# Kernel tuning notes

Hardware: AMD Instinct MI355X
Metric: run time of the kernel (lower is better)

The kernel has to match this reference:

```python
import jax, jax.numpy as jnp
import numpy as np

N_NODES = 100000
N_EDGES = 1600000
MSG_DIM = 16
HID_DIM = 16
N_ETYPE = 16
N_CLASSES = 64


def setup_inputs() -> dict:
    key = jax.random.key(0)
    ks = jax.random.split(key, 11)
    s = 1.0 / np.sqrt(HID_DIM)
    return {
        "features": jax.random.normal(ks[0], (N_NODES, HID_DIM), dtype=jnp.float32),
        "src": jax.random.randint(ks[1], (N_EDGES,), 0, N_NODES, dtype=jnp.int32),
        "dst": jax.random.randint(ks[2], (N_EDGES,), 0, N_NODES, dtype=jnp.int32),
        "e_type": jax.random.randint(ks[3], (N_EDGES,), 0, N_ETYPE, dtype=jnp.int32),
        "edge_emb": jax.random.normal(ks[4], (N_ETYPE, MSG_DIM * HID_DIM), dtype=jnp.float32),
        "W_ih": jax.random.uniform(ks[5], (3 * HID_DIM, MSG_DIM), dtype=jnp.float32, minval=-s, maxval=s),
        "W_hh": jax.random.uniform(ks[6], (3 * HID_DIM, HID_DIM), dtype=jnp.float32, minval=-s, maxval=s),
        "b_ih": jax.random.uniform(ks[7], (3 * HID_DIM,), dtype=jnp.float32, minval=-s, maxval=s),
        "b_hh": jax.random.uniform(ks[8], (3 * HID_DIM,), dtype=jnp.float32, minval=-s, maxval=s),
        "W_out": jax.random.normal(ks[9], (N_CLASSES, HID_DIM), dtype=jnp.float32) * s,
        "b_out": jax.random.normal(ks[10], (N_CLASSES,), dtype=jnp.float32) * 0.01,
    }


def reference(features, src, dst, e_type, edge_emb, W_ih, W_hh, b_ih, b_hh, W_out, b_out):
    # Per-edge message: A_e @ h_src, A_e = edge-type embedding reshaped [msg, hid]
    A = edge_emb[e_type].reshape(-1, MSG_DIM, HID_DIM)          # [E, M, H]
    msg = jnp.einsum("emh,eh->em", A, features[src])            # [E, M]
    # Sum-aggregate messages into destination nodes
    m = jax.ops.segment_sum(msg, dst, num_segments=N_NODES)     # [N, M]
    # Single-step GRU (PyTorch gate order: r, z, n)
    gx = m @ W_ih.T + b_ih                                      # [N, 3H]
    gh = features @ W_hh.T + b_hh                               # [N, 3H]
    xr, xz, xn = jnp.split(gx, 3, axis=-1)
    hr, hz, hn = jnp.split(gh, 3, axis=-1)
    r = jax.nn.sigmoid(xr + hr)
    z = jax.nn.sigmoid(xz + hz)
    n = jnp.tanh(xn + r * hn)
    h = (1.0 - z) * n + z * features                            # [N, H]
    return h @ W_out.T + b_out                                  # [N, C]
```

## Files before the change

### kernel.cpp

```cpp
#include <hip/hip_runtime.h>

#define NNODES 100000
#define NEDGES 1600000
#define HID 16
#define MSG 16
#define NTYPE 16
#define NCLS 64

#define BSH 7
#define NBK ((NNODES + 127) >> 7)
#define CHSZ 8192
#define NCH ((NEDGES + CHSZ - 1) / CHSZ)
#define M_SCAN (NBK * NCH)
#define SCH 1024
#define NSB ((M_SCAN + SCH - 1) / SCH)

#define ASTR 20
#define ATY  320

#define RECCAP 2560
#define CHUNK 16
#define NCHK ((NEDGES + CHUNK - 1) / CHUNK)
#define AGG2_BLOCKS ((NCHK + 15) / 16)

__device__ __forceinline__ float sigmoid_f(float x) {
    return 1.0f / (1.0f + __expf(-x));
}
__device__ __forceinline__ float tanh_f(float x) {
    x = fminf(fmaxf(x, -15.0f), 15.0f);
    float e = __expf(2.0f * x);
    return (e - 1.0f) / (e + 1.0f);
}

__global__ __launch_bounds__(1024) void hist_k(const int* __restrict__ dst,
                                               int* __restrict__ cntmat) {
    __shared__ int cnt[NBK];
    const int t = threadIdx.x, ch = blockIdx.x;
    for (int b = t; b < NBK; b += 1024) cnt[b] = 0;
    __syncthreads();
    #pragma unroll
    for (int k = 0; k < CHSZ / 1024; k++) {
        int e = ch * CHSZ + k * 1024 + t;
        if (e < NEDGES) atomicAdd(&cnt[dst[e] >> BSH], 1);
    }
    __syncthreads();
    for (int b = t; b < NBK; b += 1024) cntmat[b * NCH + ch] = cnt[b];
}

__global__ __launch_bounds__(256) void scan_bsum(const int* __restrict__ x,
                                                 int* __restrict__ bsum) {
    const int t = threadIdx.x;
    int base = blockIdx.x * SCH + t * 4;
    int s = 0;
    #pragma unroll
    for (int q = 0; q < 4; q++) {
        int idx = base + q;
        if (idx < M_SCAN) s += x[idx];
    }
    #pragma unroll
    for (int d = 32; d > 0; d >>= 1) s += __shfl_down(s, d, 64);
    __shared__ int ws[4];
    int lane = t & 63, w = t >> 6;
    if (lane == 0) ws[w] = s;
    __syncthreads();
    if (t == 0) bsum[blockIdx.x] = ws[0] + ws[1] + ws[2] + ws[3];
}

__global__ __launch_bounds__(256) void scan_top(int* __restrict__ bsum) {
    const int t = threadIdx.x;
    int v = (t < NSB) ? bsum[t] : 0;
    int lane = t & 63, w = t >> 6;
    int s = v;
    #pragma unroll
    for (int d = 1; d < 64; d <<= 1) {
        int u = __shfl_up(s, d, 64);
        if (lane >= d) s += u;
    }
    __shared__ int ws[4];
    if (lane == 63) ws[w] = s;
    __syncthreads();
    int base = 0;
    #pragma unroll
    for (int q = 0; q < 4; q++) if (q < w) base += ws[q];
    if (t < NSB) bsum[t] = base + s - v;
}

__global__ __launch_bounds__(256) void scan_write(const int* __restrict__ bsum,
                                                  int* __restrict__ x) {
    const int t = threadIdx.x;
    int base = blockIdx.x * SCH + t * 4;
    int v[4]; int ts = 0;
    #pragma unroll
    for (int q = 0; q < 4; q++) {
        int idx = base + q;
        v[q] = (idx < M_SCAN) ? x[idx] : 0;
        ts += v[q];
    }
    int lane = t & 63, w = t >> 6;
    int s = ts;
    #pragma unroll
    for (int d = 1; d < 64; d <<= 1) {
        int u = __shfl_up(s, d, 64);
        if (lane >= d) s += u;
    }
    __shared__ int ws[4];
    if (lane == 63) ws[w] = s;
    __syncthreads();
    int wbase = 0;
    #pragma unroll
    for (int q = 0; q < 4; q++) if (q < w) wbase += ws[q];
    int run = bsum[blockIdx.x] + wbase + (s - ts);
    #pragma unroll
    for (int q = 0; q < 4; q++) {
        int idx = base + q;
        if (idx < M_SCAN) x[idx] = run;
        run += v[q];
    }
}

__global__ __launch_bounds__(1024) void scatter_k(const int* __restrict__ src,
                                                  const int* __restrict__ dst,
                                                  const int* __restrict__ et,
                                                  const int* __restrict__ offmat,
                                                  int* __restrict__ rec) {
    __shared__ int offc[NBK];
    const int t = threadIdx.x, ch = blockIdx.x;
    for (int b = t; b < NBK; b += 1024) offc[b] = offmat[b * NCH + ch];
    __syncthreads();
    #pragma unroll
    for (int k = 0; k < CHSZ / 1024; k++) {
        int e = ch * CHSZ + k * 1024 + t;
        if (e < NEDGES) {
            int d = dst[e];
            int b = d >> BSH;
            int pos = atomicAdd(&offc[b], 1);
            rec[pos] = src[e] | (et[e] << 17) | ((d & 127) << 21);
        }
    }
}

__global__ __launch_bounds__(256) void bnd_k(const int* __restrict__ offmat,
                                             int* __restrict__ bnd) {
    int k = blockIdx.x * 256 + threadIdx.x;
    if (k < NBK) bnd[k] = offmat[k * NCH];
    if (k == NBK) bnd[k] = NEDGES;
}

__global__ __launch_bounds__(256) void sort2_k(const int* __restrict__ offmat,
                                               int* __restrict__ rec) {
    __shared__ int buf[RECCAP];
    __shared__ int cnt[128];
    __shared__ int basec[128];
    __shared__ int wtot[4];
    const int t = threadIdx.x, b = blockIdx.x;
    const int jb = offmat[b * NCH];
    const int je = (b == NBK - 1) ? NEDGES : offmat[(b + 1) * NCH];
    const int len = je - jb;
    if (len <= 0 || len > RECCAP) return;

    if (t < 128) cnt[t] = 0;
    for (int k = t; k < len; k += 256) buf[k] = rec[jb + k];
    __syncthreads();
    for (int k = t; k < len; k += 256) atomicAdd(&cnt[((unsigned)buf[k]) >> 21], 1);
    __syncthreads();
    int v = (t < 128) ? cnt[t] : 0;
    int lane = t & 63, w = t >> 6;
    int s = v;
    #pragma unroll
    for (int d = 1; d < 64; d <<= 1) {
        int u = __shfl_up(s, d, 64);
        if (lane >= d) s += u;
    }
    if (lane == 63) wtot[w] = s;
    __syncthreads();
    if (t < 128) basec[t] = s - v + (w == 1 ? wtot[0] : 0);
    __syncthreads();
    for (int k = t; k < len; k += 256) {
        int r = buf[k];
        int p = atomicAdd(&basec[((unsigned)r) >> 21], 1);
        rec[jb + p] = r;
    }
}

__device__ __forceinline__ float dot16(const float4* A, float4 f0, float4 f1,
                                       float4 f2, float4 f3) {
    float4 A0 = A[0], A1 = A[1], A2 = A[2], A3 = A[3];
    float m;
    m  = A0.x*f0.x + A0.y*f0.y + A0.z*f0.z + A0.w*f0.w;
    m += A1.x*f1.x + A1.y*f1.y + A1.z*f1.z + A1.w*f1.w;
    m += A2.x*f2.x + A2.y*f2.y + A2.z*f2.z + A2.w*f2.w;
    m += A3.x*f3.x + A3.y*f3.y + A3.z*f3.z + A3.w*f3.w;
    return m;
}

__global__ __launch_bounds__(256) void agg2_k(const float* __restrict__ feat,
                                              const int* __restrict__ rec,
                                              const int* __restrict__ bnd_g,
                                              const float* __restrict__ edge_emb,
                                              float* __restrict__ magg) {
    __shared__ float At2[NTYPE * ATY];
    __shared__ int bnd[NBK + 1];
    const int t = threadIdx.x;
    #pragma unroll
    for (int idx = t; idx < NTYPE * MSG * HID; idx += 256) {
        int ty = idx >> 8, rem = idx & 255, ii = rem >> 4, h = rem & 15;
        At2[ty * ATY + ii * ASTR + h] = edge_emb[idx];
    }
    for (int k = t; k < NBK + 1; k += 256) bnd[k] = bnd_g[k];
    __syncthreads();

    const int g = t >> 4, i = t & 15;
    const int chunk = blockIdx.x * 16 + g;
    if (chunk >= NCHK) return;
    const int j0 = chunk * CHUNK;
    const int jend = (j0 + CHUNK < NEDGES) ? j0 + CHUNK : NEDGES;

    int lo = 0, hi = NBK;
    while (hi - lo > 1) {
        int mid = (lo + hi) >> 1;
        if (bnd[mid] <= j0) lo = mid; else hi = mid;
    }
    int b = lo, bnext = bnd[b + 1];

    float macc = 0.0f;
    int cur = -1;
    int j = j0;
    while (j < jend) {
        const bool has2 = (j + 1 < jend);
        int r1 = rec[j];
        int r2 = has2 ? rec[j + 1] : r1;
        const float4* p1 = (const float4*)(feat + (size_t)(r1 & 0x1FFFF) * HID);
        const float4* p2 = (const float4*)(feat + (size_t)(r2 & 0x1FFFF) * HID);
        float4 Fa0 = p1[0], Fa1 = p1[1], Fa2 = p1[2], Fa3 = p1[3];
        float4 Fb0 = p2[0], Fb1 = p2[1], Fb2 = p2[2], Fb3 = p2[3];
        __builtin_amdgcn_sched_barrier(0);

        while (j >= bnext) { ++b; bnext = bnd[b + 1]; }
        {
            int d1  = (b << BSH) | (((unsigned)r1) >> 21);
            int ty1 = (r1 >> 17) & 15;
            float m1 = dot16((const float4*)(At2 + ty1 * ATY + i * ASTR),
                             Fa0, Fa1, Fa2, Fa3);
            if (d1 != cur) {
                if (cur >= 0) atomicAdd(&magg[(size_t)cur * MSG + i], macc);
                macc = 0.0f; cur = d1;
            }
            macc += m1;
        }
        if (has2) {
            while (j + 1 >= bnext) { ++b; bnext = bnd[b + 1]; }
            int d2  = (b << BSH) | (((unsigned)r2) >> 21);
            int ty2 = (r2 >> 17) & 15;
            float m2 = dot16((const float4*)(At2 + ty2 * ATY + i * ASTR),
                             Fb0, Fb1, Fb2, Fb3);
            if (d2 != cur) {
                atomicAdd(&magg[(size_t)cur * MSG + i], macc);
                macc = 0.0f; cur = d2;
            }
            macc += m2;
        }
        j += 2;
    }
    if (cur >= 0) atomicAdd(&magg[(size_t)cur * MSG + i], macc);
}

__global__ __launch_bounds__(256) void ggnn_edge(
    const float* __restrict__ feat,
    const int* __restrict__ src,
    const int* __restrict__ dst,
    const int* __restrict__ etype,
    const float* __restrict__ edge_emb,
    float* __restrict__ magg)
{
    __shared__ float At[NTYPE * MSG * HID];
    for (int idx = threadIdx.x; idx < NTYPE * MSG * HID; idx += 256) {
        int ty = idx >> 8, rem = idx & 255, i = rem >> 4, hh = rem & 15;
        At[(ty << 8) | (hh << 4) | i] = edge_emb[idx];
    }
    __syncthreads();
    const long long total = (long long)NEDGES * MSG;
    for (long long w = (long long)blockIdx.x * 256 + threadIdx.x; w < total;
         w += (long long)gridDim.x * 256) {
        const int e = (int)(w >> 4);
        const int i = (int)(w & 15);
        const int s = src[e];
        const int d = dst[e];
        const int ty = etype[e];
        const float4* fp = (const float4*)(feat + (size_t)s * HID);
        const float4 f0 = fp[0], f1 = fp[1], f2 = fp[2], f3 = fp[3];
        const float* a = At + (ty << 8) + i;
        float m;
        m  = a[0*16]*f0.x + a[1*16]*f0.y + a[2*16]*f0.z + a[3*16]*f0.w;
        m += a[4*16]*f1.x + a[5*16]*f1.y + a[6*16]*f1.z + a[7*16]*f1.w;
        m += a[8*16]*f2.x + a[9*16]*f2.y + a[10*16]*f2.z + a[11*16]*f2.w;
        m += a[12*16]*f3.x + a[13*16]*f3.y + a[14*16]*f3.z + a[15*16]*f3.w;
        atomicAdd(magg + (size_t)d * MSG + i, m);
    }
}

__global__ __launch_bounds__(256) void node_k(
    const float* __restrict__ feat,
    const float* __restrict__ magg,
    const float* __restrict__ W_ih,
    const float* __restrict__ W_hh,
    const float* __restrict__ b_ih,
    const float* __restrict__ b_hh,
    const float* __restrict__ W_out,
    const float* __restrict__ b_out,
    float* __restrict__ out)
{
    __shared__ float hn_s[256 * 20];
    const int t = threadIdx.x;
    const int n = blockIdx.x * 256 + t;
    if (n < NNODES) {
        float hv[HID], mv[MSG];
        const float4* hp = (const float4*)(feat + (size_t)n * HID);
        const float4* mp = (const float4*)(magg + (size_t)n * MSG);
        #pragma unroll
        for (int q = 0; q < 4; q++) {
            float4 a = hp[q];
            hv[4*q+0] = a.x; hv[4*q+1] = a.y; hv[4*q+2] = a.z; hv[4*q+3] = a.w;
            float4 c = mp[q];
            mv[4*q+0] = c.x; mv[4*q+1] = c.y; mv[4*q+2] = c.z; mv[4*q+3] = c.w;
        }
        #pragma unroll
        for (int i = 0; i < HID; i++) {
            float xr = b_ih[i], xz = b_ih[16 + i], xn = b_ih[32 + i];
            float hr = b_hh[i], hz = b_hh[16 + i], hn = b_hh[32 + i];
            #pragma unroll
            for (int j = 0; j < HID; j++) {
                xr += W_ih[(i)      * 16 + j] * mv[j];
                xz += W_ih[(16 + i) * 16 + j] * mv[j];
                xn += W_ih[(32 + i) * 16 + j] * mv[j];
                hr += W_hh[(i)      * 16 + j] * hv[j];
                hz += W_hh[(16 + i) * 16 + j] * hv[j];
                hn += W_hh[(32 + i) * 16 + j] * hv[j];
            }
            float r  = sigmoid_f(xr + hr);
            float z  = sigmoid_f(xz + hz);
            float nn = tanh_f(xn + r * hn);
            hn_s[t * 20 + i] = (1.0f - z) * nn + z * hv[i];
        }
    }
    __syncthreads();

    const int w = t >> 6, g = (t >> 4) & 3, li = t & 15;
    float4 w4[4][4];
    #pragma unroll
    for (int rr = 0; rr < 4; rr++)
        #pragma unroll
        for (int qq = 0; qq < 4; qq++)
            w4[rr][qq] = ((const float4*)W_out)[(4 * li + rr) * 4 + qq];
    const float4 bo4 = ((const float4*)b_out)[li];
    const int nb = blockIdx.x * 256;

    #pragma unroll
    for (int it = 0; it < 16; it++) {
        int ln = it * 16 + w * 4 + g;
        int n2 = nb + ln;
        if (n2 < NNODES) {
            const float4* hq = (const float4*)(hn_s + ln * 20);
            float4 h0 = hq[0], h1 = hq[1], h2 = hq[2], h3 = hq[3];
            float4 o;
            o.x = bo4.x + w4[0][0].x*h0.x + w4[0][0].y*h0.y + w4[0][0].z*h0.z + w4[0][0].w*h0.w
                        + w4[0][1].x*h1.x + w4[0][1].y*h1.y + w4[0][1].z*h1.z + w4[0][1].w*h1.w
                        + w4[0][2].x*h2.x + w4[0][2].y*h2.y + w4[0][2].z*h2.z + w4[0][2].w*h2.w
                        + w4[0][3].x*h3.x + w4[0][3].y*h3.y + w4[0][3].z*h3.z + w4[0][3].w*h3.w;
            o.y = bo4.y + w4[1][0].x*h0.x + w4[1][0].y*h0.y + w4[1][0].z*h0.z + w4[1][0].w*h0.w
                        + w4[1][1].x*h1.x + w4[1][1].y*h1.y + w4[1][1].z*h1.z + w4[1][1].w*h1.w
                        + w4[1][2].x*h2.x + w4[1][2].y*h2.y + w4[1][2].z*h2.z + w4[1][2].w*h2.w
                        + w4[1][3].x*h3.x + w4[1][3].y*h3.y + w4[1][3].z*h3.z + w4[1][3].w*h3.w;
            o.z = bo4.z + w4[2][0].x*h0.x + w4[2][0].y*h0.y + w4[2][0].z*h0.z + w4[2][0].w*h0.w
                        + w4[2][1].x*h1.x + w4[2][1].y*h1.y + w4[2][1].z*h1.z + w4[2][1].w*h1.w
                        + w4[2][2].x*h2.x + w4[2][2].y*h2.y + w4[2][2].z*h2.z + w4[2][2].w*h2.w
                        + w4[2][3].x*h3.x + w4[2][3].y*h3.y + w4[2][3].z*h3.z + w4[2][3].w*h3.w;
            o.w = bo4.w + w4[3][0].x*h0.x + w4[3][0].y*h0.y + w4[3][0].z*h0.z + w4[3][0].w*h0.w
                        + w4[3][1].x*h1.x + w4[3][1].y*h1.y + w4[3][1].z*h1.z + w4[3][1].w*h1.w
                        + w4[3][2].x*h2.x + w4[3][2].y*h2.y + w4[3][2].z*h2.z + w4[3][2].w*h2.w
                        + w4[3][3].x*h3.x + w4[3][3].y*h3.y + w4[3][3].z*h3.z + w4[3][3].w*h3.w;
            ((float4*)(out + (size_t)n2 * NCLS))[li] = o;
        }
    }
}

extern "C" void kernel_launch(void* const* d_in, const int* in_sizes, int n_in,
                              void* d_out, int out_size, void* d_ws, size_t ws_size,
                              hipStream_t stream) {
    const float* feat     = (const float*)d_in[0];
    const int*   src      = (const int*)d_in[1];
    const int*   dst      = (const int*)d_in[2];
    const int*   etype    = (const int*)d_in[3];
    const float* edge_emb = (const float*)d_in[4];
    const float* W_ih     = (const float*)d_in[5];
    const float* W_hh     = (const float*)d_in[6];
    const float* b_ih     = (const float*)d_in[7];
    const float* b_hh     = (const float*)d_in[8];
    const float* W_out    = (const float*)d_in[9];
    const float* b_out    = (const float*)d_in[10];
    float* out = (float*)d_out;

    float* magg   = (float*)d_ws;
    int*   offmat = (int*)d_ws + (size_t)NNODES * MSG;
    int*   bsum   = offmat + M_SCAN;
    int*   bnd    = bsum + 256;
    int*   rec    = bnd + 1024;
    size_t need   = ((size_t)NNODES * MSG + M_SCAN + 256 + 1024 + NEDGES) * 4;

    hipMemsetAsync(magg, 0, (size_t)NNODES * MSG * sizeof(float), stream);
    if (ws_size >= need) {
        hist_k    <<<NCH, 1024, 0, stream>>>(dst, offmat);
        scan_bsum <<<NSB, 256, 0, stream>>>(offmat, bsum);
        scan_top  <<<1, 256, 0, stream>>>(bsum);
        scan_write<<<NSB, 256, 0, stream>>>(bsum, offmat);
        scatter_k <<<NCH, 1024, 0, stream>>>(src, dst, etype, offmat, rec);
        bnd_k     <<<4, 256, 0, stream>>>(offmat, bnd);
        sort2_k   <<<NBK, 256, 0, stream>>>(offmat, rec);
        agg2_k    <<<AGG2_BLOCKS, 256, 0, stream>>>(feat, rec, bnd, edge_emb, magg);
    } else {
        ggnn_edge<<<2560, 256, 0, stream>>>(feat, src, dst, etype, edge_emb, magg);
    }
    node_k<<<(NNODES + 255) / 256, 256, 0, stream>>>(
        feat, magg, W_ih, W_hh, b_ih, b_hh, W_out, b_out, out);
}
```

Measured before the change: 158.7 us.

## Fuse scan-top and bnd kernels, precompute chunk-bucket map, stage records in LDS

Drops the single-block scan_top launch by having each scan_write block reduce the preceding block sums itself, and writes bucket boundaries there, which removes the bnd_k launch. sort2_k now also fills a chunk-to-bucket table, so agg2_k no longer copies the boundary array into shared memory or binary-searches it. agg2_k stages its 256 records in LDS and runs a fixed 8-iteration loop that assumes the edge count divides evenly by the chunk size. The cost is a redundant partial reduction in every scan block and an extra workspace array.

```diff
diff --git a/kernel.cpp b/kernel.cpp
--- a/kernel.cpp
+++ b/kernel.cpp
@@ -20,8 +20,8 @@
 
 #define RECCAP 2560
 #define CHUNK 16
-#define NCHK ((NEDGES + CHUNK - 1) / CHUNK)
-#define AGG2_BLOCKS ((NCHK + 15) / 16)
+#define NCHK (NEDGES / CHUNK)
+#define AGG2_BLOCKS (NCHK / 16)
 
 __device__ __forceinline__ float sigmoid_f(float x) {
     return 1.0f / (1.0f + __expf(-x));
@@ -66,28 +66,23 @@
     if (t == 0) bsum[blockIdx.x] = ws[0] + ws[1] + ws[2] + ws[3];
 }
 
-__global__ __launch_bounds__(256) void scan_top(int* __restrict__ bsum) {
+__global__ __launch_bounds__(256) void scan_write(const int* __restrict__ bsum,
+                                                  int* __restrict__ x,
+                                                  int* __restrict__ bnd) {
     const int t = threadIdx.x;
-    int v = (t < NSB) ? bsum[t] : 0;
-    int lane = t & 63, w = t >> 6;
-    int s = v;
-    #pragma unroll
-    for (int d = 1; d < 64; d <<= 1) {
-        int u = __shfl_up(s, d, 64);
-        if (lane >= d) s += u;
-    }
-    __shared__ int ws[4];
-    if (lane == 63) ws[w] = s;
-    __syncthreads();
-    int base = 0;
-    #pragma unroll
-    for (int q = 0; q < 4; q++) if (q < w) base += ws[q];
-    if (t < NSB) bsum[t] = base + s - v;
-}
-
-__global__ __launch_bounds__(256) void scan_write(const int* __restrict__ bsum,
-                                                  int* __restrict__ x) {
-    const int t = threadIdx.x;
+    __shared__ int wsA[4];
+    __shared__ int bpref_s;
+    {
+        int v = (t < blockIdx.x && t < NSB) ? bsum[t] : 0;
+        #pragma unroll
+        for (int d = 32; d > 0; d >>= 1) v += __shfl_down(v, d, 64);
+        int lane = t & 63, w = t >> 6;
+        if (lane == 0) wsA[w] = v;
+        __syncthreads();
+        if (t == 0) bpref_s = wsA[0] + wsA[1] + wsA[2] + wsA[3];
+        __syncthreads();
+    }
+
     int base = blockIdx.x * SCH + t * 4;
     int v[4]; int ts = 0;
     #pragma unroll
@@ -103,19 +98,23 @@
         int u = __shfl_up(s, d, 64);
         if (lane >= d) s += u;
     }
-    __shared__ int ws[4];
-    if (lane == 63) ws[w] = s;
+    __shared__ int wsB[4];
+    if (lane == 63) wsB[w] = s;
     __syncthreads();
     int wbase = 0;
     #pragma unroll
-    for (int q = 0; q < 4; q++) if (q < w) wbase += ws[q];
-    int run = bsum[blockIdx.x] + wbase + (s - ts);
+    for (int q = 0; q < 4; q++) if (q < w) wbase += wsB[q];
+    int run = bpref_s + wbase + (s - ts);
     #pragma unroll
     for (int q = 0; q < 4; q++) {
         int idx = base + q;
-        if (idx < M_SCAN) x[idx] = run;
+        if (idx < M_SCAN) {
+            x[idx] = run;
+            if (idx % NCH == 0) bnd[idx / NCH] = run;
+        }
         run += v[q];
     }
+    if (blockIdx.x == 0 && t == 0) bnd[NBK] = NEDGES;
 }
 
 __global__ __launch_bounds__(1024) void scatter_k(const int* __restrict__ src,
@@ -139,47 +138,46 @@
     }
 }
 
-__global__ __launch_bounds__(256) void bnd_k(const int* __restrict__ offmat,
-                                             int* __restrict__ bnd) {
-    int k = blockIdx.x * 256 + threadIdx.x;
-    if (k < NBK) bnd[k] = offmat[k * NCH];
-    if (k == NBK) bnd[k] = NEDGES;
-}
-
-__global__ __launch_bounds__(256) void sort2_k(const int* __restrict__ offmat,
-                                               int* __restrict__ rec) {
+__global__ __launch_bounds__(256) void sort2_k(const int* __restrict__ bnd,
+                                               int* __restrict__ rec,
+                                               int* __restrict__ cb) {
     __shared__ int buf[RECCAP];
     __shared__ int cnt[128];
     __shared__ int basec[128];
     __shared__ int wtot[4];
     const int t = threadIdx.x, b = blockIdx.x;
-    const int jb = offmat[b * NCH];
-    const int je = (b == NBK - 1) ? NEDGES : offmat[(b + 1) * NCH];
+    const int jb = bnd[b];
+    const int je = bnd[b + 1];
     const int len = je - jb;
-    if (len <= 0 || len > RECCAP) return;
-
-    if (t < 128) cnt[t] = 0;
-    for (int k = t; k < len; k += 256) buf[k] = rec[jb + k];
-    __syncthreads();
-    for (int k = t; k < len; k += 256) atomicAdd(&cnt[((unsigned)buf[k]) >> 21], 1);
-    __syncthreads();
-    int v = (t < 128) ? cnt[t] : 0;
-    int lane = t & 63, w = t >> 6;
-    int s = v;
-    #pragma unroll
-    for (int d = 1; d < 64; d <<= 1) {
-        int u = __shfl_up(s, d, 64);
-        if (lane >= d) s += u;
-    }
-    if (lane == 63) wtot[w] = s;
-    __syncthreads();
-    if (t < 128) basec[t] = s - v + (w == 1 ? wtot[0] : 0);
-    __syncthreads();
-    for (int k = t; k < len; k += 256) {
-        int r = buf[k];
-        int p = atomicAdd(&basec[((unsigned)r) >> 21], 1);
-        rec[jb + p] = r;
-    }
+
+    if (len > 0 && len <= RECCAP) {
+        if (t < 128) cnt[t] = 0;
+        for (int k = t; k < len; k += 256) buf[k] = rec[jb + k];
+        __syncthreads();
+        for (int k = t; k < len; k += 256) atomicAdd(&cnt[((unsigned)buf[k]) >> 21], 1);
+        __syncthreads();
+        int v = (t < 128) ? cnt[t] : 0;
+        int lane = t & 63, w = t >> 6;
+        int s = v;
+        #pragma unroll
+        for (int d = 1; d < 64; d <<= 1) {
+            int u = __shfl_up(s, d, 64);
+            if (lane >= d) s += u;
+        }
+        if (lane == 63) wtot[w] = s;
+        __syncthreads();
+        if (t < 128) basec[t] = s - v + (w == 1 ? wtot[0] : 0);
+        __syncthreads();
+        for (int k = t; k < len; k += 256) {
+            int r = buf[k];
+            int p = atomicAdd(&basec[((unsigned)r) >> 21], 1);
+            rec[jb + p] = r;
+        }
+    }
+
+    const int c0 = (jb + CHUNK - 1) >> 4;
+    const int c1 = (je + CHUNK - 1) >> 4;
+    for (int c = c0 + t; c < c1; c += 256) cb[c] = b;
 }
 
 __device__ __forceinline__ float dot16(const float4* A, float4 f0, float4 f1,
@@ -195,73 +193,63 @@
 
 __global__ __launch_bounds__(256) void agg2_k(const float* __restrict__ feat,
                                               const int* __restrict__ rec,
-                                              const int* __restrict__ bnd_g,
+                                              const int* __restrict__ bnd,
+                                              const int* __restrict__ cb,
                                               const float* __restrict__ edge_emb,
                                               float* __restrict__ magg) {
     __shared__ float At2[NTYPE * ATY];
-    __shared__ int bnd[NBK + 1];
+    __shared__ int recs[256];
     const int t = threadIdx.x;
     #pragma unroll
     for (int idx = t; idx < NTYPE * MSG * HID; idx += 256) {
         int ty = idx >> 8, rem = idx & 255, ii = rem >> 4, h = rem & 15;
         At2[ty * ATY + ii * ASTR + h] = edge_emb[idx];
     }
-    for (int k = t; k < NBK + 1; k += 256) bnd[k] = bnd_g[k];
+    recs[t] = rec[blockIdx.x * 256 + t];
     __syncthreads();
 
     const int g = t >> 4, i = t & 15;
     const int chunk = blockIdx.x * 16 + g;
-    if (chunk >= NCHK) return;
-    const int j0 = chunk * CHUNK;
-    const int jend = (j0 + CHUNK < NEDGES) ? j0 + CHUNK : NEDGES;
-
-    int lo = 0, hi = NBK;
-    while (hi - lo > 1) {
-        int mid = (lo + hi) >> 1;
-        if (bnd[mid] <= j0) lo = mid; else hi = mid;
-    }
-    int b = lo, bnext = bnd[b + 1];
+    const int jbase = chunk << 4;
+    const int lbase = g << 4;
+
+    int b = cb[chunk];
+    int bnext = bnd[b + 1];
 
     float macc = 0.0f;
     int cur = -1;
-    int j = j0;
-    while (j < jend) {
-        const bool has2 = (j + 1 < jend);
-        int r1 = rec[j];
-        int r2 = has2 ? rec[j + 1] : r1;
+    #pragma unroll 1
+    for (int p = 0; p < 8; p++) {
+        int r1 = recs[lbase + 2 * p];
+        int r2 = recs[lbase + 2 * p + 1];
         const float4* p1 = (const float4*)(feat + (size_t)(r1 & 0x1FFFF) * HID);
         const float4* p2 = (const float4*)(feat + (size_t)(r2 & 0x1FFFF) * HID);
         float4 Fa0 = p1[0], Fa1 = p1[1], Fa2 = p1[2], Fa3 = p1[3];
         float4 Fb0 = p2[0], Fb1 = p2[1], Fb2 = p2[2], Fb3 = p2[3];
         __builtin_amdgcn_sched_barrier(0);
 
+        int j = jbase + 2 * p;
         while (j >= bnext) { ++b; bnext = bnd[b + 1]; }
-        {
-            int d1  = (b << BSH) | (((unsigned)r1) >> 21);
-            int ty1 = (r1 >> 17) & 15;
-            float m1 = dot16((const float4*)(At2 + ty1 * ATY + i * ASTR),
-                             Fa0, Fa1, Fa2, Fa3);
-            if (d1 != cur) {
-                if (cur >= 0) atomicAdd(&magg[(size_t)cur * MSG + i], macc);
-                macc = 0.0f; cur = d1;
-            }
-            macc += m1;
-        }
-        if (has2) {
-            while (j + 1 >= bnext) { ++b; bnext = bnd[b + 1]; }
-            int d2  = (b << BSH) | (((unsigned)r2) >> 21);
-            int ty2 = (r2 >> 17) & 15;
-            float m2 = dot16((const float4*)(At2 + ty2 * ATY + i * ASTR),
-                             Fb0, Fb1, Fb2, Fb3);
-            if (d2 != cur) {
-                atomicAdd(&magg[(size_t)cur * MSG + i], macc);
-                macc = 0.0f; cur = d2;
-            }
-            macc += m2;
-        }
-        j += 2;
-    }
-    if (cur >= 0) atomicAdd(&magg[(size_t)cur * MSG + i], macc);
+        int d1 = (b << BSH) | (((unsigned)r1) >> 21);
+        float m1 = dot16((const float4*)(At2 + ((r1 >> 17) & 15) * ATY + i * ASTR),
+                         Fa0, Fa1, Fa2, Fa3);
+        if (d1 != cur) {
+            if (cur >= 0) atomicAdd(&magg[(size_t)cur * MSG + i], macc);
+            macc = 0.0f; cur = d1;
+        }
+        macc += m1;
+
+        while (j + 1 >= bnext) { ++b; bnext = bnd[b + 1]; }
+        int d2 = (b << BSH) | (((unsigned)r2) >> 21);
+        float m2 = dot16((const float4*)(At2 + ((r2 >> 17) & 15) * ATY + i * ASTR),
+                         Fb0, Fb1, Fb2, Fb3);
+        if (d2 != cur) {
+            atomicAdd(&magg[(size_t)cur * MSG + i], macc);
+            macc = 0.0f; cur = d2;
+        }
+        macc += m2;
+    }
+    atomicAdd(&magg[(size_t)cur * MSG + i], macc);
 }
 
 __global__ __launch_bounds__(256) void ggnn_edge(
@@ -403,19 +391,18 @@
     int*   offmat = (int*)d_ws + (size_t)NNODES * MSG;
     int*   bsum   = offmat + M_SCAN;
     int*   bnd    = bsum + 256;
-    int*   rec    = bnd + 1024;
-    size_t need   = ((size_t)NNODES * MSG + M_SCAN + 256 + 1024 + NEDGES) * 4;
+    int*   cb     = bnd + 1024;
+    int*   rec    = cb + NCHK;
+    size_t need   = ((size_t)NNODES * MSG + M_SCAN + 256 + 1024 + NCHK + NEDGES) * 4;
 
     hipMemsetAsync(magg, 0, (size_t)NNODES * MSG * sizeof(float), stream);
     if (ws_size >= need) {
         hist_k    <<<NCH, 1024, 0, stream>>>(dst, offmat);
         scan_bsum <<<NSB, 256, 0, stream>>>(offmat, bsum);
-        scan_top  <<<1, 256, 0, stream>>>(bsum);
-        scan_write<<<NSB, 256, 0, stream>>>(bsum, offmat);
+        scan_write<<<NSB, 256, 0, stream>>>(bsum, offmat, bnd);
         scatter_k <<<NCH, 1024, 0, stream>>>(src, dst, etype, offmat, rec);
-        bnd_k     <<<4, 256, 0, stream>>>(offmat, bnd);
-        sort2_k   <<<NBK, 256, 0, stream>>>(offmat, rec);
-        agg2_k    <<<AGG2_BLOCKS, 256, 0, stream>>>(feat, rec, bnd, edge_emb, magg);
+        sort2_k   <<<NBK, 256, 0, stream>>>(bnd, rec, cb);
+        agg2_k    <<<AGG2_BLOCKS, 256, 0, stream>>>(feat, rec, bnd, cb, edge_emb, magg);
     } else {
         ggnn_edge<<<2560, 256, 0, stream>>>(feat, src, dst, etype, edge_emb, magg);
     }
```

New measurement: 142.0 us. 10.5% less time.
